# Kernel tuning notes

Measured on AMD Instinct MI355X. Metric: run time of the kernel, lower is better.

## Reference

```python
import jax, jax.numpy as jnp
import numpy as np

IN_FEATURES = 128
HIDDEN_DIM = 128
ALPHA = 0.2
NEG_INF = -9e15


def setup_inputs() -> dict:
    key = jax.random.key(0)
    k1, k2, k3, k4, k5 = jax.random.split(key, 5)
    N, n_context = 20000, 32
    h_i = jax.random.normal(k1, (N, IN_FEATURES), dtype=jnp.float32)
    context_indices = jax.random.randint(k2, (N, n_context), 0, N, dtype=jnp.int64)
    # learned params (torch nn.Linear default init scale ~ U(-1/sqrt(fan_in), 1/sqrt(fan_in)))
    s1 = 1.0 / np.sqrt(IN_FEATURES)
    s2 = 1.0 / np.sqrt(2 * HIDDEN_DIM)
    W_i = jax.random.uniform(k3, (IN_FEATURES, HIDDEN_DIM), jnp.float32, -s1, s1)
    W_j = jax.random.uniform(k4, (IN_FEATURES, HIDDEN_DIM), jnp.float32, -s1, s1)
    ka, kb = jax.random.split(k5)
    a_w = jax.random.uniform(ka, (2 * HIDDEN_DIM, 1), jnp.float32, -s2, s2)
    a_b = jax.random.uniform(kb, (1,), jnp.float32, -s2, s2)
    return {"h_i": h_i, "context_indices": context_indices,
            "W_i": W_i, "W_j": W_j, "a_w": a_w, "a_b": a_b}


def reference(h_i, context_indices, W_i, W_j, a_w, a_b):
    N, n_context = context_indices.shape
    # -1 padding maps to an extra zero row (torch indexes -1 -> last row of padded table)
    h_padded = jnp.concatenate([h_i, jnp.zeros((1, h_i.shape[1]), h_i.dtype)], axis=0)
    idx = jnp.where(context_indices >= 0, context_indices, N)
    h_j = h_padded[idx]                      # [N, n_context, in_features]
    Wh_i = h_i @ W_i                         # [N, hidden]
    Wh_j = jnp.einsum('ncf,fh->nch', h_j, W_j)  # [N, n_context, hidden]
    # attention_layer(cat(Wh_i, Wh_j)) split into two matvecs (same math as concat)
    a_i, a_j = a_w[:HIDDEN_DIM, 0], a_w[HIDDEN_DIM:, 0]
    e = Wh_i @ a_i                           # [N]
    e = e[:, None] + Wh_j @ a_j + a_b[0]     # [N, n_context]
    e = jax.nn.leaky_relu(e, ALPHA)
    e = jnp.where(context_indices >= 0, e, NEG_INF)
    attn = jax.nn.softmax(e, axis=1)         # [N, n_context]
    h_prime = jnp.einsum('nc,nch->nh', attn, Wh_j)
    return h_prime
```

## Files before the change

### kernel.cpp

```cpp
#include <hip/hip_runtime.h>
#include <hip/hip_fp16.h>

#define GAT_ALPHA 0.2f
#define GAT_NEG_INF -9.0e15f

typedef _Float16 half8_t __attribute__((ext_vector_type(8)));
typedef float f32x4 __attribute__((ext_vector_type(4)));

__global__ __launch_bounds__(256) void gat_transform_mfma(
    const float* __restrict__ h, const float* __restrict__ Wi,
    const float* __restrict__ Wj, const float* __restrict__ aw,
    const float* __restrict__ ab,
    __half* __restrict__ Wh16, float* __restrict__ e1, float* __restrict__ e2,
    int N) {
    __shared__ _Float16 sWt[128 * 136];
    __shared__ float svi[128];
    const int t = threadIdx.x;

    if (t < 128) {
        const float4* wrow = (const float4*)(Wi + (size_t)t * 128);
        const float4* a4 = (const float4*)aw;
        float s = 0.f;
        #pragma unroll
        for (int i = 0; i < 32; ++i) {
            float4 w = wrow[i], a = a4[i];
            s = fmaf(w.x, a.x, s); s = fmaf(w.y, a.y, s);
            s = fmaf(w.z, a.z, s); s = fmaf(w.w, a.w, s);
        }
        svi[t] = s;
    }
    for (int i = t; i < 128 * 128; i += 256) {
        int k = i >> 7, n = i & 127;
        sWt[n * 136 + k] = (_Float16)Wj[i];
    }
    __syncthreads();

    const int wave = t >> 6, lane = t & 63, q = lane >> 4, l16 = lane & 15;
    const float abv = ab[0];

    float vir[4][8];
    #pragma unroll
    for (int s = 0; s < 4; ++s) {
        float4 u0 = *(const float4*)(svi + s * 32 + q * 8);
        float4 u1 = *(const float4*)(svi + s * 32 + q * 8 + 4);
        vir[s][0] = u0.x; vir[s][1] = u0.y; vir[s][2] = u0.z; vir[s][3] = u0.w;
        vir[s][4] = u1.x; vir[s][5] = u1.y; vir[s][6] = u1.z; vir[s][7] = u1.w;
    }
    float ajr[8];
    #pragma unroll
    for (int c = 0; c < 8; ++c) ajr[c] = aw[128 + c * 16 + l16];

    const int ntiles = (N + 15) >> 4;
    for (int tile = blockIdx.x * 4 + wave; tile < ntiles; tile += gridDim.x * 4) {
        const int base = tile << 4;
        int row = base + l16; if (row >= N) row = N - 1;
        const float* hp = h + (size_t)row * 128 + q * 8;

        half8_t af[4];
        float pe1 = 0.f;
        #pragma unroll
        for (int s = 0; s < 4; ++s) {
            float4 f0 = *(const float4*)(hp + s * 32);
            float4 f1 = *(const float4*)(hp + s * 32 + 4);
            pe1 = fmaf(f0.x, vir[s][0], pe1); pe1 = fmaf(f0.y, vir[s][1], pe1);
            pe1 = fmaf(f0.z, vir[s][2], pe1); pe1 = fmaf(f0.w, vir[s][3], pe1);
            pe1 = fmaf(f1.x, vir[s][4], pe1); pe1 = fmaf(f1.y, vir[s][5], pe1);
            pe1 = fmaf(f1.z, vir[s][6], pe1); pe1 = fmaf(f1.w, vir[s][7], pe1);
            half8_t a;
            a[0] = (_Float16)f0.x; a[1] = (_Float16)f0.y;
            a[2] = (_Float16)f0.z; a[3] = (_Float16)f0.w;
            a[4] = (_Float16)f1.x; a[5] = (_Float16)f1.y;
            a[6] = (_Float16)f1.z; a[7] = (_Float16)f1.w;
            af[s] = a;
        }

        f32x4 acc[8];
        #pragma unroll
        for (int c = 0; c < 8; ++c) { f32x4 z = {0.f, 0.f, 0.f, 0.f}; acc[c] = z; }

        const _Float16* wbase = sWt + l16 * 136 + q * 8;
        #pragma unroll
        for (int s = 0; s < 4; ++s) {
            #pragma unroll
            for (int c = 0; c < 8; ++c) {
                half8_t bf = *(const half8_t*)(wbase + c * (16 * 136) + s * 32);
                acc[c] = __builtin_amdgcn_mfma_f32_16x16x32_f16(af[s], bf, acc[c], 0, 0, 0);
            }
        }

        const bool full = (base + 16 <= N);
        float pe2[4] = {0.f, 0.f, 0.f, 0.f};
        #pragma unroll
        for (int c = 0; c < 8; ++c) {
            #pragma unroll
            for (int r = 0; r < 4; ++r) {
                float v = acc[c][r];
                pe2[r] = fmaf(v, ajr[c], pe2[r]);
                int rr = base + q * 4 + r;
                if (full || rr < N)
                    Wh16[(size_t)rr * 128 + (c * 16 + l16)] = __float2half(v);
            }
        }
        #pragma unroll
        for (int r = 0; r < 4; ++r) {
            pe2[r] += __shfl_xor(pe2[r], 1);
            pe2[r] += __shfl_xor(pe2[r], 2);
            pe2[r] += __shfl_xor(pe2[r], 4);
            pe2[r] += __shfl_xor(pe2[r], 8);
        }
        if (l16 == 0) {
            #pragma unroll
            for (int r = 0; r < 4; ++r) {
                int rr = base + q * 4 + r;
                if (rr < N) e2[rr] = pe2[r];
            }
        }
        pe1 += __shfl_xor(pe1, 16);
        pe1 += __shfl_xor(pe1, 32);
        if (lane < 16) {
            int rr = base + lane;
            if (rr < N) e1[rr] = pe1 + abv;
        }
    }
}

__global__ __launch_bounds__(256, 6) void gat_gather1(
    const int* __restrict__ ctx, const float* __restrict__ e1,
    const float* __restrict__ e2, const __half* __restrict__ Wh16,
    float* __restrict__ out, int N) {
    const int t = threadIdx.x;
    const int wave = t >> 6, lane = t & 63;
    const int qq = lane >> 4, ll = lane & 15;
    const int n = blockIdx.x * 4 + wave;
    if (n >= N) return;

    const int c32 = lane & 31;
    const int j = ctx[(size_t)n * 32 + c32];
    const bool v = (j >= 0);
    const int jj = v ? j : 0;
    const float eb = e1[n];

    const float e2v = e2[jj];

    const int o = jj << 8;
    const int qb = qq * 8;
    const char* wb = (const char*)Wh16 + (size_t)(ll * 16);
    const int off0 = __shfl(o, qb + 0, 32);
    const int off1 = __shfl(o, qb + 1, 32);
    const int off2 = __shfl(o, qb + 2, 32);
    const int off3 = __shfl(o, qb + 3, 32);
    const int off4 = __shfl(o, qb + 4, 32);
    const int off5 = __shfl(o, qb + 5, 32);
    const int off6 = __shfl(o, qb + 6, 32);
    const int off7 = __shfl(o, qb + 7, 32);
    half8_t hv0 = *(const half8_t*)(wb + off0);
    half8_t hv1 = *(const half8_t*)(wb + off1);
    half8_t hv2 = *(const half8_t*)(wb + off2);
    half8_t hv3 = *(const half8_t*)(wb + off3);
    half8_t hv4 = *(const half8_t*)(wb + off4);
    half8_t hv5 = *(const half8_t*)(wb + off5);
    half8_t hv6 = *(const half8_t*)(wb + off6);
    half8_t hv7 = *(const half8_t*)(wb + off7);

    float lg = eb + e2v;
    lg = fmaxf(lg, GAT_ALPHA * lg);
    lg = v ? lg : GAT_NEG_INF;
    float m = lg;
    #pragma unroll
    for (int s = 16; s; s >>= 1) m = fmaxf(m, __shfl_xor(m, s, 32));
    float p = v ? __expf(lg - m) : 0.f;
    float ss = p;
    #pragma unroll
    for (int s = 16; s; s >>= 1) ss += __shfl_xor(ss, s, 32);
    const float inv = (ss > 0.f) ? __frcp_rn(ss) : 0.f;
    p *= inv;

    const float w0 = __shfl(p, qb + 0, 32);
    const float w1 = __shfl(p, qb + 1, 32);
    const float w2 = __shfl(p, qb + 2, 32);
    const float w3 = __shfl(p, qb + 3, 32);
    const float w4 = __shfl(p, qb + 4, 32);
    const float w5 = __shfl(p, qb + 5, 32);
    const float w6 = __shfl(p, qb + 6, 32);
    const float w7 = __shfl(p, qb + 7, 32);

    float a0 = 0.f, a1 = 0.f, a2 = 0.f, a3 = 0.f;
    float a4 = 0.f, a5 = 0.f, a6 = 0.f, a7 = 0.f;
#define GAT_ACC(HV, W)                                                   \
    a0 = fmaf(W, (float)HV[0], a0); a1 = fmaf(W, (float)HV[1], a1);      \
    a2 = fmaf(W, (float)HV[2], a2); a3 = fmaf(W, (float)HV[3], a3);      \
    a4 = fmaf(W, (float)HV[4], a4); a5 = fmaf(W, (float)HV[5], a5);      \
    a6 = fmaf(W, (float)HV[6], a6); a7 = fmaf(W, (float)HV[7], a7);
    GAT_ACC(hv0, w0) GAT_ACC(hv1, w1) GAT_ACC(hv2, w2) GAT_ACC(hv3, w3)
    GAT_ACC(hv4, w4) GAT_ACC(hv5, w5) GAT_ACC(hv6, w6) GAT_ACC(hv7, w7)
#undef GAT_ACC

    a0 += __shfl_xor(a0, 16); a1 += __shfl_xor(a1, 16);
    a2 += __shfl_xor(a2, 16); a3 += __shfl_xor(a3, 16);
    a4 += __shfl_xor(a4, 16); a5 += __shfl_xor(a5, 16);
    a6 += __shfl_xor(a6, 16); a7 += __shfl_xor(a7, 16);
    a0 += __shfl_xor(a0, 32); a1 += __shfl_xor(a1, 32);
    a2 += __shfl_xor(a2, 32); a3 += __shfl_xor(a3, 32);
    a4 += __shfl_xor(a4, 32); a5 += __shfl_xor(a5, 32);
    a6 += __shfl_xor(a6, 32); a7 += __shfl_xor(a7, 32);

    if (lane < 16) {
        float4* orow = (float4*)(out + (size_t)n * 128);
        float4 u; u.x = a0; u.y = a1; u.z = a2; u.w = a3;
        float4 w2v; w2v.x = a4; w2v.y = a5; w2v.z = a6; w2v.w = a7;
        orow[2 * ll] = u;
        orow[2 * ll + 1] = w2v;
    }
}

extern "C" void kernel_launch(void* const* d_in, const int* in_sizes, int n_in,
                              void* d_out, int out_size, void* d_ws, size_t ws_size,
                              hipStream_t stream) {
    const float* h   = (const float*)d_in[0];
    const int*   ctx = (const int*)d_in[1];
    const float* Wi  = (const float*)d_in[2];
    const float* Wj  = (const float*)d_in[3];
    const float* aw  = (const float*)d_in[4];
    const float* ab  = (const float*)d_in[5];
    float* out = (float*)d_out;
    const int N = in_sizes[0] / 128;

    float* e1 = (float*)d_ws;
    float* e2 = e1 + N;
    __half* Wh16 = (__half*)(e2 + N);

    const int ntiles = (N + 15) >> 4;
    const int g1 = (ntiles + 3) / 4;
    const int g2 = (N + 3) / 4;

    gat_transform_mfma<<<g1, 256, 0, stream>>>(h, Wi, Wj, aw, ab, Wh16, e1, e2, N);
    gat_gather1<<<g2, 256, 0, stream>>>(ctx, e1, e2, Wh16, out, N);
}
```

Baseline: 102.3 us.

## Split Wh into two 64-column planes and gather each in a separate pass

```diff
diff --git a/kernel.cpp b/kernel.cpp
--- a/kernel.cpp
+++ b/kernel.cpp
@@ -5,14 +5,15 @@
 #define GAT_NEG_INF -9.0e15f
 
 typedef _Float16 half8_t __attribute__((ext_vector_type(8)));
+typedef _Float16 half4_t __attribute__((ext_vector_type(4)));
 typedef float f32x4 __attribute__((ext_vector_type(4)));
 
 __global__ __launch_bounds__(256) void gat_transform_mfma(
     const float* __restrict__ h, const float* __restrict__ Wi,
     const float* __restrict__ Wj, const float* __restrict__ aw,
     const float* __restrict__ ab,
-    __half* __restrict__ Wh16, float* __restrict__ e1, float* __restrict__ e2,
-    int N) {
+    __half* __restrict__ Wh0, __half* __restrict__ Wh1,
+    float* __restrict__ e1, float* __restrict__ e2, int N) {
     __shared__ _Float16 sWt[128 * 136];
     __shared__ float svi[128];
     const int t = threadIdx.x;
@@ -92,13 +93,15 @@
         float pe2[4] = {0.f, 0.f, 0.f, 0.f};
         #pragma unroll
         for (int c = 0; c < 8; ++c) {
+            __half* dst = (c < 4) ? Wh0 : Wh1;
+            const int c64 = (c & 3) * 16 + l16;
             #pragma unroll
             for (int r = 0; r < 4; ++r) {
                 float v = acc[c][r];
                 pe2[r] = fmaf(v, ajr[c], pe2[r]);
                 int rr = base + q * 4 + r;
                 if (full || rr < N)
-                    Wh16[(size_t)rr * 128 + (c * 16 + l16)] = __float2half(v);
+                    dst[(size_t)rr * 64 + c64] = __float2half(v);
             }
         }
         #pragma unroll
@@ -124,10 +127,10 @@
     }
 }
 
-__global__ __launch_bounds__(256, 6) void gat_gather1(
+__global__ __launch_bounds__(256, 8) void gat_gather_plane(
     const int* __restrict__ ctx, const float* __restrict__ e1,
-    const float* __restrict__ e2, const __half* __restrict__ Wh16,
-    float* __restrict__ out, int N) {
+    const float* __restrict__ e2, const __half* __restrict__ plane,
+    float* __restrict__ out, int N, int dbase) {
     const int t = threadIdx.x;
     const int wave = t >> 6, lane = t & 63;
     const int qq = lane >> 4, ll = lane & 15;
@@ -135,16 +138,16 @@
     if (n >= N) return;
 
     const int c32 = lane & 31;
-    const int j = ctx[(size_t)n * 32 + c32];
+    const int j = __builtin_nontemporal_load(ctx + (size_t)n * 32 + c32);
     const bool v = (j >= 0);
     const int jj = v ? j : 0;
     const float eb = e1[n];
 
     const float e2v = e2[jj];
 
-    const int o = jj << 8;
+    const int o = jj << 7;
     const int qb = qq * 8;
-    const char* wb = (const char*)Wh16 + (size_t)(ll * 16);
+    const char* wb = (const char*)plane + (size_t)(ll * 8);
     const int off0 = __shfl(o, qb + 0, 32);
     const int off1 = __shfl(o, qb + 1, 32);
     const int off2 = __shfl(o, qb + 2, 32);
@@ -153,14 +156,14 @@
     const int off5 = __shfl(o, qb + 5, 32);
     const int off6 = __shfl(o, qb + 6, 32);
     const int off7 = __shfl(o, qb + 7, 32);
-    half8_t hv0 = *(const half8_t*)(wb + off0);
-    half8_t hv1 = *(const half8_t*)(wb + off1);
-    half8_t hv2 = *(const half8_t*)(wb + off2);
-    half8_t hv3 = *(const half8_t*)(wb + off3);
-    half8_t hv4 = *(const half8_t*)(wb + off4);
-    half8_t hv5 = *(const half8_t*)(wb + off5);
-    half8_t hv6 = *(const half8_t*)(wb + off6);
-    half8_t hv7 = *(const half8_t*)(wb + off7);
+    half4_t hv0 = *(const half4_t*)(wb + off0);
+    half4_t hv1 = *(const half4_t*)(wb + off1);
+    half4_t hv2 = *(const half4_t*)(wb + off2);
+    half4_t hv3 = *(const half4_t*)(wb + off3);
+    half4_t hv4 = *(const half4_t*)(wb + off4);
+    half4_t hv5 = *(const half4_t*)(wb + off5);
+    half4_t hv6 = *(const half4_t*)(wb + off6);
+    half4_t hv7 = *(const half4_t*)(wb + off7);
 
     float lg = eb + e2v;
     lg = fmaxf(lg, GAT_ALPHA * lg);
@@ -185,31 +188,22 @@
     const float w7 = __shfl(p, qb + 7, 32);
 
     float a0 = 0.f, a1 = 0.f, a2 = 0.f, a3 = 0.f;
-    float a4 = 0.f, a5 = 0.f, a6 = 0.f, a7 = 0.f;
 #define GAT_ACC(HV, W)                                                   \
     a0 = fmaf(W, (float)HV[0], a0); a1 = fmaf(W, (float)HV[1], a1);      \
-    a2 = fmaf(W, (float)HV[2], a2); a3 = fmaf(W, (float)HV[3], a3);      \
-    a4 = fmaf(W, (float)HV[4], a4); a5 = fmaf(W, (float)HV[5], a5);      \
-    a6 = fmaf(W, (float)HV[6], a6); a7 = fmaf(W, (float)HV[7], a7);
+    a2 = fmaf(W, (float)HV[2], a2); a3 = fmaf(W, (float)HV[3], a3);
     GAT_ACC(hv0, w0) GAT_ACC(hv1, w1) GAT_ACC(hv2, w2) GAT_ACC(hv3, w3)
     GAT_ACC(hv4, w4) GAT_ACC(hv5, w5) GAT_ACC(hv6, w6) GAT_ACC(hv7, w7)
 #undef GAT_ACC
 
     a0 += __shfl_xor(a0, 16); a1 += __shfl_xor(a1, 16);
     a2 += __shfl_xor(a2, 16); a3 += __shfl_xor(a3, 16);
-    a4 += __shfl_xor(a4, 16); a5 += __shfl_xor(a5, 16);
-    a6 += __shfl_xor(a6, 16); a7 += __shfl_xor(a7, 16);
     a0 += __shfl_xor(a0, 32); a1 += __shfl_xor(a1, 32);
     a2 += __shfl_xor(a2, 32); a3 += __shfl_xor(a3, 32);
-    a4 += __shfl_xor(a4, 32); a5 += __shfl_xor(a5, 32);
-    a6 += __shfl_xor(a6, 32); a7 += __shfl_xor(a7, 32);
 
     if (lane < 16) {
-        float4* orow = (float4*)(out + (size_t)n * 128);
-        float4 u; u.x = a0; u.y = a1; u.z = a2; u.w = a3;
-        float4 w2v; w2v.x = a4; w2v.y = a5; w2v.z = a6; w2v.w = a7;
-        orow[2 * ll] = u;
-        orow[2 * ll + 1] = w2v;
+        f32x4 u; u[0] = a0; u[1] = a1; u[2] = a2; u[3] = a3;
+        f32x4* orow = (f32x4*)(out + (size_t)n * 128 + dbase) + ll;
+        __builtin_nontemporal_store(u, orow);
     }
 }
 
@@ -227,12 +221,14 @@
 
     float* e1 = (float*)d_ws;
     float* e2 = e1 + N;
-    __half* Wh16 = (__half*)(e2 + N);
+    __half* Wh0 = (__half*)(e2 + N);
+    __half* Wh1 = Wh0 + (size_t)N * 64;
 
     const int ntiles = (N + 15) >> 4;
     const int g1 = (ntiles + 3) / 4;
     const int g2 = (N + 3) / 4;
 
-    gat_transform_mfma<<<g1, 256, 0, stream>>>(h, Wi, Wj, aw, ab, Wh16, e1, e2, N);
-    gat_gather1<<<g2, 256, 0, stream>>>(ctx, e1, e2, Wh16, out, N);
+    gat_transform_mfma<<<g1, 256, 0, stream>>>(h, Wi, Wj, aw, ab, Wh0, Wh1, e1, e2, N);
+    gat_gather_plane<<<g2, 256, 0, stream>>>(ctx, e1, e2, Wh0, out, N, 0);
+    gat_gather_plane<<<g2, 256, 0, stream>>>(ctx, e1, e2, Wh1, out, N, 64);
 }
```

New measurement: 107.2 us. 4.8% more time.
